# Performance work log

Hardware: AMD Instinct MI355X
Metric: run time of the kernel (lower is better)

Reference implementation:

```python
import jax, jax.numpy as jnp
import numpy as np

K = 16        # neighbors (init kwarg k)
LN_EPS = 1e-5


def setup_inputs() -> dict:
    key = jax.random.key(0)
    ks = jax.random.split(key, 12)
    B, N, C, H = 4, 4096, 64, 12
    w = lambda k, s: jax.random.normal(k, s, jnp.float32) * 0.05
    d = {}
    d["x"] = jax.random.normal(ks[0], (B, N, C), jnp.float32)
    d["pos"] = jax.random.uniform(ks[1], (B, N, 3), jnp.float32)
    # to_q / to_k / to_v (bias=False). Stored as [in,out]; apply as x @ W.
    d["Wq"] = w(ks[2], (C, C)); d["Wk"] = w(ks[3], (C, C)); d["Wv"] = w(ks[4], (C, C))
    # pos_mlp: Linear(3,H) -> LayerNorm(H) -> ReLU -> Linear(H,C)
    d["p_w1"] = w(ks[5], (3, H)); d["p_b1"] = jnp.zeros((H,), jnp.float32)
    d["p_g"] = jnp.ones((H,), jnp.float32); d["p_be"] = jnp.zeros((H,), jnp.float32)
    d["p_w2"] = w(ks[6], (H, C)); d["p_b2"] = jnp.zeros((C,), jnp.float32)
    # attn_mlp: Linear(C,C) -> LayerNorm(C) -> ReLU -> Linear(C,C)
    d["a_w1"] = w(ks[7], (C, C)); d["a_b1"] = jnp.zeros((C,), jnp.float32)
    d["a_g"] = jnp.ones((C,), jnp.float32); d["a_be"] = jnp.zeros((C,), jnp.float32)
    d["a_w2"] = w(ks[8], (C, C)); d["a_b2"] = jnp.zeros((C,), jnp.float32)
    return d


def _ln(x, g, b):
    m = x.mean(-1, keepdims=True)
    v = ((x - m) ** 2).mean(-1, keepdims=True)
    return (x - m) * jax.lax.rsqrt(v + LN_EPS) * g + b


def _gather(feats, idx):
    # feats [B,N,C], idx [B,N,K] -> [B,N,K,C]
    return jax.vmap(lambda f, i: f[i])(feats, idx)


def reference(x, pos, Wq, Wk, Wv, p_w1, p_b1, p_g, p_be, p_w2, p_b2,
              a_w1, a_b1, a_g, a_be, a_w2, a_b2):
    # knn_points(pos, pos, K, return_sorted=True): K nearest by squared dist
    sq = jnp.sum(pos * pos, axis=-1)                       # [B,N]
    d2 = sq[:, :, None] + sq[:, None, :] - 2.0 * jnp.einsum('bnd,bmd->bnm', pos, pos)
    _, idx = jax.lax.top_k(-d2, K)                         # [B,N,K], ascending distance
    knn_xyz = _gather(pos, idx)                            # [B,N,K,3]
    q = x @ Wq                                             # [B,N,C]
    k = _gather(x @ Wk, idx)                               # [B,N,K,C]
    v = _gather(x @ Wv, idx)                               # [B,N,K,C]
    rel = pos[:, :, None, :] - knn_xyz                     # [B,N,K,3]
    pos_enc = jax.nn.relu(_ln(rel @ p_w1 + p_b1, p_g, p_be)) @ p_w2 + p_b2   # [B,N,K,C]
    w_in = q[:, :, None, :] - k + pos_enc                  # [B,N,K,C]
    attn = jax.nn.relu(_ln(w_in @ a_w1 + a_b1, a_g, a_be)) @ a_w2 + a_b2
    attn = jax.nn.softmax(attn, axis=-2)                   # softmax over K neighbors
    return jnp.einsum('bikd,bikd->bid', attn, v + pos_enc) # [B,N,C]
```

## Files before the change

kernel.cpp:

```cpp
#include <hip/hip_runtime.h>
#include <math.h>

#define NPTS 4096
#define KNN 16
#define LN_EPS 1e-5f

#define BOOT 128
#define CAP0 32
#define TRIG 24
#define CAP1 72
#define C1S  928
#define CHSZ 1056
#define SEG  352


__global__ __launch_bounds__(256) void proj3_kernel(
    const float* __restrict__ x, const float* __restrict__ Wq,
    const float* __restrict__ Wk, const float* __restrict__ Wv,
    float* __restrict__ qf, float* __restrict__ kf, float* __restrict__ vf) {
  int g = blockIdx.x * 256 + threadIdx.x;
  int r = g >> 6, c = g & 63;
  float sq = 0.f, sk = 0.f, sv = 0.f;
  for (int i = 0; i < 64; ++i) {
    float xv = x[r*64 + i];
    sq += xv * Wq[i*64 + c];
    sk += xv * Wk[i*64 + c];
    sv += xv * Wv[i*64 + c];
  }
  qf[g] = sq; kf[g] = sk; vf[g] = sv;
}

#define INSERT_CHAIN(DD, JJ)                                          \
  do {                                                                \
    float dd = (DD); int jj = (JJ);                                   \
    _Pragma("unroll")                                                 \
    for (int v = 0; v < 16; ++v) {                                    \
      bool sw = dd < ld[v];                                           \
      float nd = sw ? dd : ld[v]; float td = sw ? ld[v] : dd;         \
      int   nj = sw ? jj : lj[v]; int   tj = sw ? lj[v] : jj;         \
      ld[v] = nd; lj[v] = nj; dd = td; jj = tj;                       \
    }                                                                 \
  } while (0)

#define REPLAY0()                                                     \
  do {                                                                \
    for (int i = 0; ; ++i) {                                          \
      unsigned long long alive = __ballot(i < cnt);                   \
      if (!alive) break;                                              \
      if (i < cnt) {                                                  \
        float dd0 = s_buf0[i*128 + bo];                               \
        int   jj0 = __float_as_int(s_buf0[i*128 + bo + 1]);           \
        if (dd0 < ld[15]) INSERT_CHAIN(dd0, jj0);                     \
      }                                                               \
    }                                                                 \
    cnt = 0; thr = ld[15]; s_thr[tid] = thr;                          \
  } while (0)

#define GROUP_D2(SBASE)                                               \
  float4 p[8];                                                        \
  _Pragma("unroll")                                                   \
  for (int u = 0; u < 8; ++u) p[u] = s_p[(SBASE) + u];                \
  float d2v[8];                                                       \
  _Pragma("unroll")                                                   \
  for (int u = 0; u < 8; ++u) {                                       \
    float acc = __fmul_rn(qx, p[u].x);                                \
    acc = __fmaf_rn(qy, p[u].y, acc);                                 \
    acc = __fmaf_rn(qz, p[u].z, acc);                                 \
    d2v[u] = __fsub_rn(__fadd_rn(sqn, p[u].w), __fmul_rn(2.0f, acc)); \
  }

#define TREE_OFFS(THRV)                                               \
  int f0 = (d2v[0] < (THRV)) ? 1 : 0, f1 = (d2v[1] < (THRV)) ? 1 : 0, \
      f2 = (d2v[2] < (THRV)) ? 1 : 0, f3 = (d2v[3] < (THRV)) ? 1 : 0, \
      f4 = (d2v[4] < (THRV)) ? 1 : 0, f5 = (d2v[5] < (THRV)) ? 1 : 0, \
      f6 = (d2v[6] < (THRV)) ? 1 : 0, f7 = (d2v[7] < (THRV)) ? 1 : 0; \
  int s01 = f0+f1, s23 = f2+f3, s45 = f4+f5, s67 = f6+f7;             \
  int s03 = s01+s23, s47 = s45+s67;                                   \
  int o[8];                                                           \
  o[0] = cnt;        o[1] = cnt + f0;   o[2] = cnt + s01;             \
  o[3] = cnt + s01 + f2;                o[4] = cnt + s03;             \
  o[5] = o[4] + f4;  o[6] = o[4] + s45; o[7] = o[6] + f6;

__global__ __launch_bounds__(256) void knn_gated4_kernel(
    const float* __restrict__ pos, int* __restrict__ idx_out) {
  __shared__ __align__(16) float4 s_p[NPTS];
  __shared__ __align__(16) float  s_buf0[CAP0*128];
  __shared__ int   s_j1[3][(CAP1+1)*64];
  __shared__ float s_thr[64];
  __shared__ int   s_cnt1[3][64];
  __shared__ int   s_gen;
  __shared__ int   s_ovf;

  int t = threadIdx.x;
  int tid = t & 63, w = t >> 6, b = blockIdx.y;
  const float* pb = pos + b*NPTS*3;
  for (int j = t; j < NPTS; j += 256) {
    float px = pb[j*3+0], py = pb[j*3+1], pz = pb[j*3+2];
    float sq = __fadd_rn(__fadd_rn(__fmul_rn(px,px), __fmul_rn(py,py)),
                         __fmul_rn(pz,pz));
    s_p[j] = make_float4(px, py, pz, sq);
  }
  if (t < 64) s_thr[t] = INFINITY;
  if (t == 0) { s_ovf = 0; s_gen = 0; }
  __syncthreads();

  int n = blockIdx.x * 64 + tid;
  float4 qp = s_p[n];
  float qx = qp.x, qy = qp.y, qz = qp.z, sqn = qp.w;
  float ld[16]; int lj[16];
#pragma unroll
  for (int u = 0; u < 16; ++u) { ld[u] = INFINITY; lj[u] = 0x7fffffff; }

  for (int s = 0; s < BOOT; s += 8) {
    GROUP_D2(s)
#pragma unroll
    for (int u = 0; u < 8; ++u) {
      float d2 = d2v[u];
      if (d2 < ld[15]) INSERT_CHAIN(d2, s + u);
    }
  }
  float thr = ld[15];
  int bo = tid << 1;
  int cnt = 0;

  if (w == 0) {
    for (int s = BOOT; s < C1S; s += 8) {
      GROUP_D2(s)
      TREE_OFFS(thr)
#pragma unroll
      for (int u = 0; u < 8; ++u) {
        s_buf0[o[u]*128 + bo]     = d2v[u];
        s_buf0[o[u]*128 + bo + 1] = __int_as_float(s + u);
      }
      cnt += s03 + s47;
      int done = s + 8;
      bool pub = ((done & 127) == 0) && done >= 256 && done <= 896;
      if (pub || __ballot(cnt >= TRIG) != 0ULL) {
        REPLAY0();
        if (pub) {
          __threadfence_block();
          s_gen = (done >> 7) - 1;
        }
      }
    }
    REPLAY0();
    __syncthreads();

    int ovf = s_ovf;
    for (int ch = 0; ch < 3; ++ch) {
      int cs = C1S + ch*CHSZ;
      if (ovf & (1 << ch)) {
        int ce = cs + CHSZ;
        for (int s = cs; s < ce; s += 8) {
          GROUP_D2(s)
          TREE_OFFS(thr)
#pragma unroll
          for (int u = 0; u < 8; ++u) {
            s_buf0[o[u]*128 + bo]     = d2v[u];
            s_buf0[o[u]*128 + bo + 1] = __int_as_float(s + u);
          }
          cnt += s03 + s47;
          if (__ballot(cnt >= TRIG) != 0ULL) REPLAY0();
        }
        REPLAY0();
      } else {
        const int* jb = &s_j1[ch][0];
        int cc = s_cnt1[ch][tid];
        int jn = (0 < cc) ? jb[tid] : 0;
        float4 pn = s_p[jn];
        for (int i = 0; ; ++i) {
          unsigned long long alive = __ballot(i < cc);
          if (!alive) break;
          int jj0 = jn; float4 pj = pn;
          int ix = i + 1;
          jn = (ix < cc) ? jb[ix*64 + tid] : 0;
          pn = s_p[jn];
          if (i < cc) {
            float acc = __fmul_rn(qx, pj.x);
            acc = __fmaf_rn(qy, pj.y, acc);
            acc = __fmaf_rn(qz, pj.z, acc);
            float dd0 = __fsub_rn(__fadd_rn(sqn, pj.w), __fmul_rn(2.0f, acc));
            if (dd0 < ld[15]) INSERT_CHAIN(dd0, jj0);
          }
        }
      }
    }
    int* outp = idx_out + (b*NPTS + n)*KNN;
#pragma unroll
    for (int u = 0; u < 16; ++u) outp[u] = b*NPTS + lj[u];
  } else {
    int cs = C1S + (w-1)*CHSZ;
    int* jb = &s_j1[w-1][0];
    float thrW = thr;
#pragma unroll
    for (int seg = 0; seg < 3; ++seg) {
      int need = 2*seg + 2;
      while (*((volatile int*)&s_gen) < need) __builtin_amdgcn_s_sleep(2);
      thrW = fminf(thrW, *((volatile float*)&s_thr[tid]));
      int ss = cs + seg*SEG, se = ss + SEG;
      for (int s = ss; s < se; s += 8) {
        GROUP_D2(s)
        TREE_OFFS(thrW)
#pragma unroll
        for (int u = 0; u < 8; ++u) {
          int oc = (o[u] <= CAP1) ? o[u] : CAP1;
          jb[oc*64 + tid] = s + u;
        }
        cnt += s03 + s47;
      }
    }
    s_cnt1[w-1][tid] = (cnt <= CAP1) ? cnt : CAP1;
    if (cnt > CAP1) atomicOr(&s_ovf, 1 << (w-1));
    __syncthreads();
  }
}

__device__ __forceinline__ float wsum64(float v) {
  v += __shfl_xor(v, 1);
  v += __shfl_xor(v, 2);
  v += __shfl_xor(v, 4);
  v += __shfl_xor(v, 8);
  v += __shfl_xor(v, 16);
  v += __shfl_xor(v, 32);
  return v;
}

__device__ __forceinline__ float bcast(float v, int lane) {
  return __int_as_float(__builtin_amdgcn_readlane(__float_as_int(v), lane));
}

__global__ __launch_bounds__(256) void fuse_kernel(
    const float* __restrict__ pos, const int* __restrict__ idx,
    const float* __restrict__ qf, const float* __restrict__ kf,
    const float* __restrict__ vf,
    const float* __restrict__ p_w1, const float* __restrict__ p_b1,
    const float* __restrict__ p_g, const float* __restrict__ p_be,
    const float* __restrict__ p_w2, const float* __restrict__ p_b2,
    const float* __restrict__ a_w1, const float* __restrict__ a_b1,
    const float* __restrict__ a_g, const float* __restrict__ a_be,
    const float* __restrict__ a_w2, const float* __restrict__ a_b2,
    float* __restrict__ out) {
  __shared__ int   s_j[16];
  __shared__ float s_h[16][12];
  __shared__ __align__(16) float s_ve[16][64];
  __shared__ __align__(16) float s_t2[16][64];
  __shared__ float s_pw2[768];
  __shared__ __align__(16) float s_w1t[64][64];
  __shared__ __align__(16) float s_w2t[64][64];

  int tid = threadIdx.x;
  int p = blockIdx.x;
  int c = tid & 63, kq = tid >> 6;

  for (int e = tid; e < 4096; e += 256) {
    int i = e >> 6, cc = e & 63;
    int g = i >> 2, go = i & 3;
    int gs = g ^ (cc & 15);
    s_w1t[cc][4*gs + go] = a_w1[e];
    s_w2t[cc][4*gs + go] = a_w2[e];
  }
  for (int e = tid; e < 768; e += 256) s_pw2[e] = p_w2[e];

  if (tid < 16) {
    int j = idx[p*KNN + tid];
    s_j[tid] = j;
    float rx = pos[p*3+0] - pos[j*3+0];
    float ry = pos[p*3+1] - pos[j*3+1];
    float rz = pos[p*3+2] - pos[j*3+2];
    float hv[12];
    float mean = 0.f;
#pragma unroll
    for (int h = 0; h < 12; ++h) {
      float v = rx*p_w1[h] + ry*p_w1[12+h] + rz*p_w1[24+h] + p_b1[h];
      hv[h] = v; mean += v;
    }
    mean *= (1.0f/12.0f);
    float var = 0.f;
#pragma unroll
    for (int h = 0; h < 12; ++h) { float d = hv[h] - mean; var += d*d; }
    var *= (1.0f/12.0f);
    float rs = rsqrtf(var + LN_EPS);
#pragma unroll
    for (int h = 0; h < 12; ++h) {
      float a = (hv[h] - mean)*rs*p_g[h] + p_be[h];
      s_h[tid][h] = fmaxf(a, 0.f);
    }
  }
  __syncthreads();

  float win0, win1, win2, win3;
  {
    float qv = qf[p*64 + c];
    float pb2 = p_b2[c];
    float pe0 = pb2, pe1 = pb2, pe2 = pb2, pe3 = pb2;
#pragma unroll
    for (int h = 0; h < 12; ++h) {
      float wv = s_pw2[h*64 + c];
      pe0 = __fmaf_rn(s_h[kq][h],    wv, pe0);
      pe1 = __fmaf_rn(s_h[4+kq][h],  wv, pe1);
      pe2 = __fmaf_rn(s_h[8+kq][h],  wv, pe2);
      pe3 = __fmaf_rn(s_h[12+kq][h], wv, pe3);
    }
    int j0 = s_j[kq], j1 = s_j[4+kq], j2 = s_j[8+kq], j3 = s_j[12+kq];
    win0 = qv - kf[j0*64 + c] + pe0;  s_ve[kq][c]    = vf[j0*64 + c] + pe0;
    win1 = qv - kf[j1*64 + c] + pe1;  s_ve[4+kq][c]  = vf[j1*64 + c] + pe1;
    win2 = qv - kf[j2*64 + c] + pe2;  s_ve[8+kq][c]  = vf[j2*64 + c] + pe2;
    win3 = qv - kf[j3*64 + c] + pe3;  s_ve[12+kq][c] = vf[j3*64 + c] + pe3;
  }

  int swz = c & 15;
  float wcol[64];

  {
    const float* w1r = &s_w1t[c][0];
#pragma unroll
    for (int ii = 0; ii < 16; ++ii) {
      float4 wa = *(const float4*)(w1r + 4*(ii ^ swz));
      wcol[4*ii+0] = wa.x; wcol[4*ii+1] = wa.y;
      wcol[4*ii+2] = wa.z; wcol[4*ii+3] = wa.w;
    }
  }
  float ab1 = a_b1[c];
  float a0 = ab1, a1 = ab1, a2 = ab1, a3 = ab1;
#pragma unroll
  for (int i = 0; i < 64; ++i) {
    float b0 = bcast(win0, i), b1 = bcast(win1, i);
    float b2 = bcast(win2, i), b3 = bcast(win3, i);
    a0 = __fmaf_rn(b0, wcol[i], a0);
    a1 = __fmaf_rn(b1, wcol[i], a1);
    a2 = __fmaf_rn(b2, wcol[i], a2);
    a3 = __fmaf_rn(b3, wcol[i], a3);
  }

  float ag = a_g[c], abe = a_be[c];
  float r0, r1, r2, r3;
  {
    float m = wsum64(a0) * (1.0f/64.0f); float d = a0 - m;
    float var = wsum64(d*d) * (1.0f/64.0f);
    r0 = fmaxf(d*rsqrtf(var + LN_EPS)*ag + abe, 0.f);
  }
  {
    float m = wsum64(a1) * (1.0f/64.0f); float d = a1 - m;
    float var = wsum64(d*d) * (1.0f/64.0f);
    r1 = fmaxf(d*rsqrtf(var + LN_EPS)*ag + abe, 0.f);
  }
  {
    float m = wsum64(a2) * (1.0f/64.0f); float d = a2 - m;
    float var = wsum64(d*d) * (1.0f/64.0f);
    r2 = fmaxf(d*rsqrtf(var + LN_EPS)*ag + abe, 0.f);
  }
  {
    float m = wsum64(a3) * (1.0f/64.0f); float d = a3 - m;
    float var = wsum64(d*d) * (1.0f/64.0f);
    r3 = fmaxf(d*rsqrtf(var + LN_EPS)*ag + abe, 0.f);
  }

  {
    const float* w2r = &s_w2t[c][0];
#pragma unroll
    for (int ii = 0; ii < 16; ++ii) {
      float4 wa = *(const float4*)(w2r + 4*(ii ^ swz));
      wcol[4*ii+0] = wa.x; wcol[4*ii+1] = wa.y;
      wcol[4*ii+2] = wa.z; wcol[4*ii+3] = wa.w;
    }
  }
  float ab2 = a_b2[c];
  float t0 = ab2, t1 = ab2, t2 = ab2, t3 = ab2;
#pragma unroll
  for (int i = 0; i < 64; ++i) {
    float b0 = bcast(r0, i), b1 = bcast(r1, i);
    float b2 = bcast(r2, i), b3 = bcast(r3, i);
    t0 = __fmaf_rn(b0, wcol[i], t0);
    t1 = __fmaf_rn(b1, wcol[i], t1);
    t2 = __fmaf_rn(b2, wcol[i], t2);
    t3 = __fmaf_rn(b3, wcol[i], t3);
  }
  s_t2[kq][c]    = t0;
  s_t2[4+kq][c]  = t1;
  s_t2[8+kq][c]  = t2;
  s_t2[12+kq][c] = t3;
  __syncthreads();

  if (tid < 64) {
    float mx = -INFINITY;
    for (int k = 0; k < 16; ++k) mx = fmaxf(mx, s_t2[k][tid]);
    float se = 0.f, po = 0.f;
    for (int k = 0; k < 16; ++k) {
      float e = expf(s_t2[k][tid] - mx);
      se += e; po += e * s_ve[k][tid];
    }
    out[p*64 + tid] = po / se;
  }
}

extern "C" void kernel_launch(void* const* d_in, const int* in_sizes, int n_in,
                              void* d_out, int out_size, void* d_ws, size_t ws_size,
                              hipStream_t stream) {
  const float* x    = (const float*)d_in[0];
  const float* pos  = (const float*)d_in[1];
  const float* Wq   = (const float*)d_in[2];
  const float* Wk   = (const float*)d_in[3];
  const float* Wv   = (const float*)d_in[4];
  const float* p_w1 = (const float*)d_in[5];
  const float* p_b1 = (const float*)d_in[6];
  const float* p_g  = (const float*)d_in[7];
  const float* p_be = (const float*)d_in[8];
  const float* p_w2 = (const float*)d_in[9];
  const float* p_b2 = (const float*)d_in[10];
  const float* a_w1 = (const float*)d_in[11];
  const float* a_b1 = (const float*)d_in[12];
  const float* a_g  = (const float*)d_in[13];
  const float* a_be = (const float*)d_in[14];
  const float* a_w2 = (const float*)d_in[15];
  const float* a_b2 = (const float*)d_in[16];

  float* ws   = (float*)d_ws;
  float* qf   = ws;
  float* kf   = qf + 1048576;
  float* vf   = kf + 1048576;
  int*   idx  = (int*)(vf + 1048576);
  float* outp = (float*)d_out;

  hipLaunchKernelGGL(proj3_kernel, dim3(4096), dim3(256), 0, stream,
                     x, Wq, Wk, Wv, qf, kf, vf);
  hipLaunchKernelGGL(knn_gated4_kernel, dim3(64, 4), dim3(256), 0, stream,
                     pos, idx);
  hipLaunchKernelGGL(fuse_kernel, dim3(16384), dim3(256), 0, stream,
                     pos, idx, qf, kf, vf,
                     p_w1, p_b1, p_g, p_be, p_w2, p_b2,
                     a_w1, a_b1, a_g, a_be, a_w2, a_b2, outp);
}
```

Baseline: 489.0 us.

## Pre-transpose attn MLP weights once and stream them from global in fuse kernel

Adds a small kernel that transposes a_w1 and a_w2 into a workspace once per call. The fuse kernel drops its per-block 32KB shared-memory staging of both weight matrices and instead reads float4 columns straight from global/L2 inside the matmul loops, and sets launch bounds to 6 blocks per CU. The aim is to remove the redundant per-block weight load and its LDS footprint, which limited occupancy, at the cost of more global/cache traffic per lane.

After: 529.5 us. 8.3% more time.

```diff
diff --git a/kernel.cpp b/kernel.cpp
--- a/kernel.cpp
+++ b/kernel.cpp
@@ -28,6 +28,15 @@
     sv += xv * Wv[i*64 + c];
   }
   qf[g] = sq; kf[g] = sk; vf[g] = sv;
+}
+
+__global__ __launch_bounds__(256) void wtrans_kernel(
+    const float* __restrict__ a_w1, const float* __restrict__ a_w2,
+    float* __restrict__ w1t, float* __restrict__ w2t) {
+  int e = blockIdx.x * 256 + threadIdx.x;
+  int i = e >> 6, c = e & 63;
+  w1t[c*64 + i] = a_w1[e];
+  w2t[c*64 + i] = a_w2[e];
 }
 
 #define INSERT_CHAIN(DD, JJ)                                          \
@@ -229,36 +238,27 @@
   return __int_as_float(__builtin_amdgcn_readlane(__float_as_int(v), lane));
 }
 
-__global__ __launch_bounds__(256) void fuse_kernel(
+__global__ __launch_bounds__(256, 6) void fuse_kernel(
     const float* __restrict__ pos, const int* __restrict__ idx,
     const float* __restrict__ qf, const float* __restrict__ kf,
     const float* __restrict__ vf,
     const float* __restrict__ p_w1, const float* __restrict__ p_b1,
     const float* __restrict__ p_g, const float* __restrict__ p_be,
     const float* __restrict__ p_w2, const float* __restrict__ p_b2,
-    const float* __restrict__ a_w1, const float* __restrict__ a_b1,
+    const float* __restrict__ w1t, const float* __restrict__ a_b1,
     const float* __restrict__ a_g, const float* __restrict__ a_be,
-    const float* __restrict__ a_w2, const float* __restrict__ a_b2,
+    const float* __restrict__ w2t, const float* __restrict__ a_b2,
     float* __restrict__ out) {
   __shared__ int   s_j[16];
   __shared__ float s_h[16][12];
   __shared__ __align__(16) float s_ve[16][64];
   __shared__ __align__(16) float s_t2[16][64];
   __shared__ float s_pw2[768];
-  __shared__ __align__(16) float s_w1t[64][64];
-  __shared__ __align__(16) float s_w2t[64][64];
 
   int tid = threadIdx.x;
   int p = blockIdx.x;
   int c = tid & 63, kq = tid >> 6;
 
-  for (int e = tid; e < 4096; e += 256) {
-    int i = e >> 6, cc = e & 63;
-    int g = i >> 2, go = i & 3;
-    int gs = g ^ (cc & 15);
-    s_w1t[cc][4*gs + go] = a_w1[e];
-    s_w2t[cc][4*gs + go] = a_w2[e];
-  }
   for (int e = tid; e < 768; e += 256) s_pw2[e] = p_w2[e];
 
   if (tid < 16) {
@@ -308,28 +308,23 @@
     win3 = qv - kf[j3*64 + c] + pe3;  s_ve[12+kq][c] = vf[j3*64 + c] + pe3;
   }
 
-  int swz = c & 15;
-  float wcol[64];
-
-  {
-    const float* w1r = &s_w1t[c][0];
-#pragma unroll
-    for (int ii = 0; ii < 16; ++ii) {
-      float4 wa = *(const float4*)(w1r + 4*(ii ^ swz));
-      wcol[4*ii+0] = wa.x; wcol[4*ii+1] = wa.y;
-      wcol[4*ii+2] = wa.z; wcol[4*ii+3] = wa.w;
-    }
-  }
+  const float* w1c = w1t + c*64;
   float ab1 = a_b1[c];
   float a0 = ab1, a1 = ab1, a2 = ab1, a3 = ab1;
 #pragma unroll
-  for (int i = 0; i < 64; ++i) {
-    float b0 = bcast(win0, i), b1 = bcast(win1, i);
-    float b2 = bcast(win2, i), b3 = bcast(win3, i);
-    a0 = __fmaf_rn(b0, wcol[i], a0);
-    a1 = __fmaf_rn(b1, wcol[i], a1);
-    a2 = __fmaf_rn(b2, wcol[i], a2);
-    a3 = __fmaf_rn(b3, wcol[i], a3);
+  for (int ii = 0; ii < 16; ++ii) {
+    float4 wa = *(const float4*)(w1c + 4*ii);
+#pragma unroll
+    for (int q = 0; q < 4; ++q) {
+      int i = 4*ii + q;
+      float wv = (q == 0) ? wa.x : (q == 1) ? wa.y : (q == 2) ? wa.z : wa.w;
+      float b0 = bcast(win0, i), b1 = bcast(win1, i);
+      float b2 = bcast(win2, i), b3 = bcast(win3, i);
+      a0 = __fmaf_rn(b0, wv, a0);
+      a1 = __fmaf_rn(b1, wv, a1);
+      a2 = __fmaf_rn(b2, wv, a2);
+      a3 = __fmaf_rn(b3, wv, a3);
+    }
   }
 
   float ag = a_g[c], abe = a_be[c];
@@ -355,25 +350,23 @@
     r3 = fmaxf(d*rsqrtf(var + LN_EPS)*ag + abe, 0.f);
   }
 
-  {
-    const float* w2r = &s_w2t[c][0];
-#pragma unroll
-    for (int ii = 0; ii < 16; ++ii) {
-      float4 wa = *(const float4*)(w2r + 4*(ii ^ swz));
-      wcol[4*ii+0] = wa.x; wcol[4*ii+1] = wa.y;
-      wcol[4*ii+2] = wa.z; wcol[4*ii+3] = wa.w;
-    }
-  }
+  const float* w2c = w2t + c*64;
   float ab2 = a_b2[c];
   float t0 = ab2, t1 = ab2, t2 = ab2, t3 = ab2;
 #pragma unroll
-  for (int i = 0; i < 64; ++i) {
-    float b0 = bcast(r0, i), b1 = bcast(r1, i);
-    float b2 = bcast(r2, i), b3 = bcast(r3, i);
-    t0 = __fmaf_rn(b0, wcol[i], t0);
-    t1 = __fmaf_rn(b1, wcol[i], t1);
-    t2 = __fmaf_rn(b2, wcol[i], t2);
-    t3 = __fmaf_rn(b3, wcol[i], t3);
+  for (int ii = 0; ii < 16; ++ii) {
+    float4 wa = *(const float4*)(w2c + 4*ii);
+#pragma unroll
+    for (int q = 0; q < 4; ++q) {
+      int i = 4*ii + q;
+      float wv = (q == 0) ? wa.x : (q == 1) ? wa.y : (q == 2) ? wa.z : wa.w;
+      float b0 = bcast(r0, i), b1 = bcast(r1, i);
+      float b2 = bcast(r2, i), b3 = bcast(r3, i);
+      t0 = __fmaf_rn(b0, wv, t0);
+      t1 = __fmaf_rn(b1, wv, t1);
+      t2 = __fmaf_rn(b2, wv, t2);
+      t3 = __fmaf_rn(b3, wv, t3);
+    }
   }
   s_t2[kq][c]    = t0;
   s_t2[4+kq][c]  = t1;
@@ -419,8 +412,12 @@
   float* kf   = qf + 1048576;
   float* vf   = kf + 1048576;
   int*   idx  = (int*)(vf + 1048576);
+  float* w1t  = (float*)(idx + 262144);
+  float* w2t  = w1t + 4096;
   float* outp = (float*)d_out;
 
+  hipLaunchKernelGGL(wtrans_kernel, dim3(16), dim3(256), 0, stream,
+                     a_w1, a_w2, w1t, w2t);
   hipLaunchKernelGGL(proj3_kernel, dim3(4096), dim3(256), 0, stream,
                      x, Wq, Wk, Wv, qf, kf, vf);
   hipLaunchKernelGGL(knn_gated4_kernel, dim3(64, 4), dim3(256), 0, stream,
@@ -428,5 +425,5 @@
   hipLaunchKernelGGL(fuse_kernel, dim3(16384), dim3(256), 0, stream,
                      pos, idx, qf, kf, vf,
                      p_w1, p_b1, p_g, p_be, p_w2, p_b2,
-                     a_w1, a_b1, a_g, a_be, a_w2, a_b2, outp);
-}
+                     w1t, a_b1, a_g, a_be, w2t, a_b2, outp);
+}
```
